# Kernel optimization log

Hardware: AMD Instinct MI355X
Metric: run time of the kernel (lower is better)

## Reference

```python
import jax, jax.numpy as jnp
import numpy as np

STATE_DIM, ACTION_DIM, HIDDEN_DIM = 12, 4, 16  # hidden_dim must equal state_dim+action_dim
LN_EPS = 1e-5


def setup_inputs() -> dict:
    key = jax.random.key(0)
    ks = jax.random.split(key, 12)
    B, T = 8192, 256
    D = STATE_DIM + ACTION_DIM  # 16
    H = HIDDEN_DIM
    s = 1.0 / np.sqrt(D)
    sh = 1.0 / np.sqrt(H)
    return {
        "initial_state": jax.random.normal(ks[0], (B, 1, STATE_DIM), jnp.float32),
        "commands": jax.random.normal(ks[1], (B, T, ACTION_DIM), jnp.float32),
        "ln_gamma": jnp.ones((D,), jnp.float32),
        "ln_beta": jnp.zeros((D,), jnp.float32),
        "W_in": jax.random.uniform(ks[2], (H, D), jnp.float32, -s, s),
        "b_in": jax.random.uniform(ks[3], (H,), jnp.float32, -s, s),
        "W_ih": jax.random.uniform(ks[4], (4 * H, D), jnp.float32, -sh, sh),  # LSTM input_size = D
        "W_hh": jax.random.uniform(ks[5], (4 * H, H), jnp.float32, -sh, sh),
        "b_ih": jax.random.uniform(ks[6], (4 * H,), jnp.float32, -sh, sh),
        "b_hh": jax.random.uniform(ks[7], (4 * H,), jnp.float32, -sh, sh),
        "W_out": jax.random.uniform(ks[8], (STATE_DIM, H), jnp.float32, -sh, sh),
        "b_out": jax.random.uniform(ks[9], (STATE_DIM,), jnp.float32, -sh, sh),
    }


def _normalize_sincos(state, cos_idx, sin_idx):
    sn, cs = state[:, sin_idx], state[:, cos_idx]
    norm = jnp.sqrt(sn * sn + cs * cs) + 1e-8
    return state.at[:, sin_idx].set(sn / norm).at[:, cos_idx].set(cs / norm)


def _forward(initial_state, commands, ln_gamma, ln_beta, W_in, b_in,
             W_ih, W_hh, b_ih, b_hh, W_out, b_out):
    B = initial_state.shape[0]
    H = W_hh.shape[1]
    state0 = initial_state[:, 0, :]  # (B, S)
    h0 = jnp.zeros((B, H), initial_state.dtype)
    c0 = jnp.zeros((B, H), initial_state.dtype)

    def step(carry, cmd_t):
        state, h, c = carry
        x = jnp.concatenate([state, cmd_t], axis=-1)          # (B, D)
        mu = jnp.mean(x, axis=-1, keepdims=True)
        var = jnp.mean((x - mu) ** 2, axis=-1, keepdims=True)
        x = (x - mu) * jax.lax.rsqrt(var + LN_EPS) * ln_gamma + ln_beta
        x = x @ W_in.T + b_in                                  # (B, H)
        gates = x @ W_ih.T + b_ih + h @ W_hh.T + b_hh          # (B, 4H)
        i, f, g, o = jnp.split(gates, 4, axis=-1)
        c = jax.nn.sigmoid(f) * c + jax.nn.sigmoid(i) * jnp.tanh(g)
        h = jax.nn.sigmoid(o) * jnp.tanh(c)
        state = state + h @ W_out.T + b_out                    # (B, S)
        state = _normalize_sincos(state, 1, 2)
        state = _normalize_sincos(state, 3, 4)
        state = _normalize_sincos(state, 5, 6)
        return (state, h, c), state

    _, outs = jax.lax.scan(step, (state0, h0, c0), jnp.swapaxes(commands, 0, 1))
    return jnp.swapaxes(outs, 0, 1)  # (B, T, S)


def reference(initial_state, commands, ln_gamma, ln_beta, W_in, b_in,
              W_ih, W_hh, b_ih, b_hh, W_out, b_out):
    return _forward(initial_state, commands, ln_gamma, ln_beta, W_in, b_in,
                    W_ih, W_hh, b_ih, b_hh, W_out, b_out)
```

## Files before the change

### kernel.cpp

```cpp
#include <hip/hip_runtime.h>

typedef float f32x2 __attribute__((ext_vector_type(2)));
typedef float f32x4 __attribute__((ext_vector_type(4)));

#define LOG2E 1.44269504088896340736f

__device__ __forceinline__ float rcp_fast(float x) { return __builtin_amdgcn_rcpf(x); }

__device__ __forceinline__ f32x2 mk2(float a, float b) { f32x2 v; v[0] = a; v[1] = b; return v; }

__device__ __forceinline__ float sigmoid_fast(float x) {
    return rcp_fast(1.0f + __builtin_amdgcn_exp2f(-LOG2E * x));
}

__device__ __forceinline__ float tanh_fast(float x) {
    float a = __builtin_fabsf(x);
    float t = __builtin_amdgcn_exp2f(-2.0f * LOG2E * a);
    float r = (1.0f - t) * rcp_fast(1.0f + t);
    return __builtin_copysignf(r, x);
}

__device__ __forceinline__ void load_pairs16(const float* p, f32x2* dst) {
    const f32x4* q4 = (const f32x4*)p;
    f32x4 a = q4[0], b = q4[1], c = q4[2], d = q4[3];
    dst[0] = __builtin_shufflevector(a, a, 0, 1);
    dst[1] = __builtin_shufflevector(a, a, 2, 3);
    dst[2] = __builtin_shufflevector(b, b, 0, 1);
    dst[3] = __builtin_shufflevector(b, b, 2, 3);
    dst[4] = __builtin_shufflevector(c, c, 0, 1);
    dst[5] = __builtin_shufflevector(c, c, 2, 3);
    dst[6] = __builtin_shufflevector(d, d, 0, 1);
    dst[7] = __builtin_shufflevector(d, d, 2, 3);
}

__global__ __launch_bounds__(64) void vm_kernel(
    const float* __restrict__ init_state,
    const float* __restrict__ commands,
    const float* __restrict__ ln_g,
    const float* __restrict__ ln_b,
    const float* __restrict__ W_in,
    const float* __restrict__ b_in,
    const float* __restrict__ W_ih,
    const float* __restrict__ W_hh,
    const float* __restrict__ b_ih,
    const float* __restrict__ b_hh,
    const float* __restrict__ W_out,
    const float* __restrict__ b_out,
    float* __restrict__ out,
    int B, int T)
{
    const int lane = threadIdx.x;
    const int j = lane & 15;
    const int g = lane >> 4;
    const int b = blockIdx.x * 4 + g;

    __shared__ float sh_x[4][20];
    __shared__ float sh_xhh[4][36];
    __shared__ float sh_hn[4][20];

    f32x2 Wg2[8];
    float wbeta;
    float sWg = 0.0f;
    {
        const float* wr = W_in + j * 16;
        float bsum = b_in[j];
        float ssum = 0.0f;
#pragma unroll
        for (int k2 = 0; k2 < 8; ++k2) {
            float w0 = wr[2 * k2], w1 = wr[2 * k2 + 1];
            float g0 = ln_g[2 * k2], g1 = ln_g[2 * k2 + 1];
            float a0 = w0 * g0, a1 = w1 * g1;
            Wg2[k2] = mk2(a0, a1);
            bsum += w0 * ln_b[2 * k2] + w1 * ln_b[2 * k2 + 1];
            ssum += a0 + a1;
        }
        wbeta = bsum;
        sWg = ssum;
    }

    f32x2 Wx[4][8], Wh[4][8];
    float gb[4];
#pragma unroll
    for (int q = 0; q < 4; ++q) {
        const float* rx = W_ih + (q * 16 + j) * 16;
        const float* rh = W_hh + (q * 16 + j) * 16;
#pragma unroll
        for (int k2 = 0; k2 < 8; ++k2) {
            Wx[q][k2] = mk2(rx[2 * k2], rx[2 * k2 + 1]);
            Wh[q][k2] = mk2(rh[2 * k2], rh[2 * k2 + 1]);
        }
        gb[q] = b_ih[q * 16 + j] + b_hh[q * 16 + j];
    }

    f32x2 Wo[8];
    float bo = 0.0f;
#pragma unroll
    for (int k2 = 0; k2 < 8; ++k2) Wo[k2] = mk2(0.0f, 0.0f);
    if (j < 12) {
        const float* ro = W_out + j * 16;
#pragma unroll
        for (int k2 = 0; k2 < 8; ++k2) Wo[k2] = mk2(ro[2 * k2], ro[2 * k2 + 1]);
        bo = b_out[j];
    }

    const bool is_state = (j < 12);
    float st = is_state ? init_state[b * 12 + j] : 0.0f;
    float h = 0.0f, c = 0.0f;

    const float* cmd_ptr = commands + (size_t)b * T * 4 + (j - 12);
    float cmd = (j >= 12) ? cmd_ptr[0] : 0.0f;

    float* out_ptr = out + (size_t)b * T * 12 + j;

    int pj = j;
    if (j >= 1 && j <= 6) pj = ((j - 1) ^ 1) + 1;
    const int psrc = (lane & 48) | pj;
    const bool donorm = (j >= 1 && j <= 6);

    for (int t = 0; t < T; ++t) {
        float x = is_state ? st : cmd;
        sh_x[g][j] = x;

        float cmd_next = 0.0f;
        {
            int tn = (t + 1 < T) ? (t + 1) : t;
            if (j >= 12) cmd_next = cmd_ptr[(size_t)tn * 4];
        }
        __syncthreads();

        f32x2 xp[8];
        load_pairs16(&sh_x[g][0], xp);

        f32x2 s2 = ((xp[0] + xp[1]) + (xp[2] + xp[3])) + ((xp[4] + xp[5]) + (xp[6] + xp[7]));
        float sum = s2[0] + s2[1];
        f32x2 q2 = xp[0] * xp[0];
#pragma unroll
        for (int k2 = 1; k2 < 8; ++k2) q2 += xp[k2] * xp[k2];
        float sumsq = q2[0] + q2[1];
        float mu = sum * 0.0625f;
        float var = sumsq * 0.0625f - mu * mu;
        float inv = __builtin_amdgcn_rsqf(var + 1e-5f);

        f32x2 d2 = Wg2[0] * xp[0];
#pragma unroll
        for (int k2 = 1; k2 < 8; ++k2) d2 += Wg2[k2] * xp[k2];
        float xh = ((d2[0] + d2[1]) - mu * sWg) * inv + wbeta;

        sh_xhh[g][j] = xh;
        sh_xhh[g][16 + j] = h;
        __syncthreads();

        f32x2 ap[8], hp[8];
        load_pairs16(&sh_xhh[g][0], ap);
        load_pairs16(&sh_xhh[g][16], hp);

        f32x2 ai = mk2(0.f, 0.f), af = mk2(0.f, 0.f), ag = mk2(0.f, 0.f), ao = mk2(0.f, 0.f);
#pragma unroll
        for (int k2 = 0; k2 < 8; ++k2) {
            f32x2 xv = ap[k2], hv = hp[k2];
            ai += Wx[0][k2] * xv; af += Wx[1][k2] * xv;
            ag += Wx[2][k2] * xv; ao += Wx[3][k2] * xv;
            ai += Wh[0][k2] * hv; af += Wh[1][k2] * hv;
            ag += Wh[2][k2] * hv; ao += Wh[3][k2] * hv;
        }
        float gi = ai[0] + ai[1] + gb[0];
        float gf = af[0] + af[1] + gb[1];
        float gg = ag[0] + ag[1] + gb[2];
        float go = ao[0] + ao[1] + gb[3];

        float iv = sigmoid_fast(gi);
        float fv = sigmoid_fast(gf);
        float gv = tanh_fast(gg);
        float ov = sigmoid_fast(go);
        c = fv * c + iv * gv;
        h = ov * tanh_fast(c);

        sh_hn[g][j] = h;
        __syncthreads();

        f32x2 hn[8];
        load_pairs16(&sh_hn[g][0], hn);
        f32x2 o2 = Wo[0] * hn[0];
#pragma unroll
        for (int k2 = 1; k2 < 8; ++k2) o2 += Wo[k2] * hn[k2];

        if (is_state) st += (o2[0] + o2[1]) + bo;

        float pv = __shfl(st, psrc, 64);
        if (donorm) {
            float n = __builtin_amdgcn_sqrtf(st * st + pv * pv) + 1e-8f;
            st *= rcp_fast(n);
        }

        if (is_state) out_ptr[0] = st;
        out_ptr += 12;
        cmd = cmd_next;
    }
}

extern "C" void kernel_launch(void* const* d_in, const int* in_sizes, int n_in,
                              void* d_out, int out_size, void* d_ws, size_t ws_size,
                              hipStream_t stream) {
    const float* init_state = (const float*)d_in[0];
    const float* commands   = (const float*)d_in[1];
    const float* ln_g       = (const float*)d_in[2];
    const float* ln_b       = (const float*)d_in[3];
    const float* W_in       = (const float*)d_in[4];
    const float* b_in       = (const float*)d_in[5];
    const float* W_ih       = (const float*)d_in[6];
    const float* W_hh       = (const float*)d_in[7];
    const float* b_ih       = (const float*)d_in[8];
    const float* b_hh       = (const float*)d_in[9];
    const float* W_out      = (const float*)d_in[10];
    const float* b_out      = (const float*)d_in[11];

    int B = in_sizes[0] / 12;
    int T = in_sizes[1] / (B * 4);

    int blocks = B / 4;
    vm_kernel<<<blocks, 64, 0, stream>>>(init_state, commands, ln_g, ln_b,
                                         W_in, b_in, W_ih, W_hh, b_ih, b_hh,
                                         W_out, b_out, (float*)d_out, B, T);
}
```

Baseline: 359.2 us.

## Replace LDS exchanges and barriers with DPP row-rotate broadcasts in LSTM step

Each batch row's 16 lanes now exchange x, h and the normalized state through DPP row_ror operations instead of shared memory plus three __syncthreads per timestep. Weights are pre-permuted per lane by the rotation index, and the input and recurrent weights are packed into f32x2 pairs so each rotation step feeds packed FMAs. This targets the per-step LDS round trips and barrier latency on the serial recurrence, at the cost of 15 DPP moves per exchange and more register pressure. Launch bounds also request 2 waves per EU.

```diff
diff --git a/kernel.cpp b/kernel.cpp
--- a/kernel.cpp
+++ b/kernel.cpp
@@ -1,13 +1,11 @@
 #include <hip/hip_runtime.h>
+#include <utility>
 
 typedef float f32x2 __attribute__((ext_vector_type(2)));
-typedef float f32x4 __attribute__((ext_vector_type(4)));
 
 #define LOG2E 1.44269504088896340736f
 
 __device__ __forceinline__ float rcp_fast(float x) { return __builtin_amdgcn_rcpf(x); }
-
-__device__ __forceinline__ f32x2 mk2(float a, float b) { f32x2 v; v[0] = a; v[1] = b; return v; }
 
 __device__ __forceinline__ float sigmoid_fast(float x) {
     return rcp_fast(1.0f + __builtin_amdgcn_exp2f(-LOG2E * x));
@@ -20,20 +18,29 @@
     return __builtin_copysignf(r, x);
 }
 
-__device__ __forceinline__ void load_pairs16(const float* p, f32x2* dst) {
-    const f32x4* q4 = (const f32x4*)p;
-    f32x4 a = q4[0], b = q4[1], c = q4[2], d = q4[3];
-    dst[0] = __builtin_shufflevector(a, a, 0, 1);
-    dst[1] = __builtin_shufflevector(a, a, 2, 3);
-    dst[2] = __builtin_shufflevector(b, b, 0, 1);
-    dst[3] = __builtin_shufflevector(b, b, 2, 3);
-    dst[4] = __builtin_shufflevector(c, c, 0, 1);
-    dst[5] = __builtin_shufflevector(c, c, 2, 3);
-    dst[6] = __builtin_shufflevector(d, d, 0, 1);
-    dst[7] = __builtin_shufflevector(d, d, 2, 3);
-}
-
-__global__ __launch_bounds__(64) void vm_kernel(
+template <int R>
+__device__ __forceinline__ int ror16_i(int v) {
+    if constexpr (R == 0) {
+        return v;
+    } else {
+        return __builtin_amdgcn_update_dpp(v, v, 0x120 + R, 0xF, 0xF, false);
+    }
+}
+template <int R>
+__device__ __forceinline__ float ror16(float v) {
+    return __builtin_bit_cast(float, ror16_i<R>(__builtin_bit_cast(int, v)));
+}
+
+template <typename F, int... Rs>
+__device__ __forceinline__ void sf_impl(F&& f, std::integer_sequence<int, Rs...>) {
+    (f(std::integral_constant<int, Rs>{}), ...);
+}
+template <int N, typename F>
+__device__ __forceinline__ void static_for(F&& f) {
+    sf_impl(f, std::make_integer_sequence<int, N>{});
+}
+
+__global__ __launch_bounds__(64, 2) void vm_kernel(
     const float* __restrict__ init_state,
     const float* __restrict__ commands,
     const float* __restrict__ ln_g,
@@ -51,57 +58,64 @@
 {
     const int lane = threadIdx.x;
     const int j = lane & 15;
-    const int g = lane >> 4;
-    const int b = blockIdx.x * 4 + g;
-
-    __shared__ float sh_x[4][20];
-    __shared__ float sh_xhh[4][36];
-    __shared__ float sh_hn[4][20];
-
-    f32x2 Wg2[8];
-    float wbeta;
-    float sWg = 0.0f;
+    const int b = blockIdx.x * 4 + (lane >> 4);
+
+    int kr[16];
+    kr[0] = j;
+    static_for<15>([&](auto rc) {
+        constexpr int R = decltype(rc)::value + 1;
+        kr[R] = ror16_i<R>(j);
+    });
+
+    float Wg[16];
+    float wbeta, sWg = 0.0f;
     {
         const float* wr = W_in + j * 16;
         float bsum = b_in[j];
-        float ssum = 0.0f;
-#pragma unroll
-        for (int k2 = 0; k2 < 8; ++k2) {
-            float w0 = wr[2 * k2], w1 = wr[2 * k2 + 1];
-            float g0 = ln_g[2 * k2], g1 = ln_g[2 * k2 + 1];
-            float a0 = w0 * g0, a1 = w1 * g1;
-            Wg2[k2] = mk2(a0, a1);
-            bsum += w0 * ln_b[2 * k2] + w1 * ln_b[2 * k2 + 1];
-            ssum += a0 + a1;
+#pragma unroll
+        for (int r = 0; r < 16; ++r) {
+            int k = kr[r];
+            float w = wr[k] * ln_g[k];
+            Wg[r] = w;
+            sWg += w;
         }
+#pragma unroll
+        for (int k = 0; k < 16; ++k) bsum += wr[k] * ln_b[k];
         wbeta = bsum;
-        sWg = ssum;
-    }
-
-    f32x2 Wx[4][8], Wh[4][8];
+    }
+
+    f32x2 Wpk[4][16];
     float gb[4];
 #pragma unroll
     for (int q = 0; q < 4; ++q) {
         const float* rx = W_ih + (q * 16 + j) * 16;
         const float* rh = W_hh + (q * 16 + j) * 16;
 #pragma unroll
-        for (int k2 = 0; k2 < 8; ++k2) {
-            Wx[q][k2] = mk2(rx[2 * k2], rx[2 * k2 + 1]);
-            Wh[q][k2] = mk2(rh[2 * k2], rh[2 * k2 + 1]);
+        for (int r = 0; r < 16; ++r) {
+            int k = kr[r];
+            f32x2 w;
+            w[0] = rx[k];
+            w[1] = rh[k];
+            Wpk[q][r] = w;
         }
         gb[q] = b_ih[q * 16 + j] + b_hh[q * 16 + j];
     }
 
-    f32x2 Wo[8];
+    float Wo[16];
     float bo = 0.0f;
 #pragma unroll
-    for (int k2 = 0; k2 < 8; ++k2) Wo[k2] = mk2(0.0f, 0.0f);
+    for (int r = 0; r < 16; ++r) Wo[r] = 0.0f;
     if (j < 12) {
         const float* ro = W_out + j * 16;
 #pragma unroll
-        for (int k2 = 0; k2 < 8; ++k2) Wo[k2] = mk2(ro[2 * k2], ro[2 * k2 + 1]);
+        for (int r = 0; r < 16; ++r) Wo[r] = ro[kr[r]];
         bo = b_out[j];
     }
+
+    int pj = j;
+    if (j >= 1 && j <= 6) pj = ((j - 1) ^ 1) + 1;
+    const bool donorm = (j >= 1 && j <= 6);
+    const bool use_r1 = (kr[1] == pj);
 
     const bool is_state = (j < 12);
     float st = is_state ? init_state[b * 12 + j] : 0.0f;
@@ -112,83 +126,68 @@
 
     float* out_ptr = out + (size_t)b * T * 12 + j;
 
-    int pj = j;
-    if (j >= 1 && j <= 6) pj = ((j - 1) ^ 1) + 1;
-    const int psrc = (lane & 48) | pj;
-    const bool donorm = (j >= 1 && j <= 6);
-
     for (int t = 0; t < T; ++t) {
         float x = is_state ? st : cmd;
-        sh_x[g][j] = x;
-
-        float cmd_next = 0.0f;
-        {
-            int tn = (t + 1 < T) ? (t + 1) : t;
-            if (j >= 12) cmd_next = cmd_ptr[(size_t)tn * 4];
-        }
-        __syncthreads();
-
-        f32x2 xp[8];
-        load_pairs16(&sh_x[g][0], xp);
-
-        f32x2 s2 = ((xp[0] + xp[1]) + (xp[2] + xp[3])) + ((xp[4] + xp[5]) + (xp[6] + xp[7]));
-        float sum = s2[0] + s2[1];
-        f32x2 q2 = xp[0] * xp[0];
-#pragma unroll
-        for (int k2 = 1; k2 < 8; ++k2) q2 += xp[k2] * xp[k2];
-        float sumsq = q2[0] + q2[1];
+
+        int tn = (t + 1 < T) ? (t + 1) : t;
+        float cmd_next = (j >= 12) ? cmd_ptr[(size_t)tn * 4] : 0.0f;
+
+        float sum = x;
+        float sumsq = x * x;
+        float dot = Wg[0] * x;
+        static_for<15>([&](auto rc) {
+            constexpr int R = decltype(rc)::value + 1;
+            float xr = ror16<R>(x);
+            sum += xr;
+            sumsq = __builtin_fmaf(xr, xr, sumsq);
+            dot = __builtin_fmaf(Wg[R], xr, dot);
+        });
         float mu = sum * 0.0625f;
-        float var = sumsq * 0.0625f - mu * mu;
+        float var = __builtin_fmaf(sumsq, 0.0625f, -mu * mu);
         float inv = __builtin_amdgcn_rsqf(var + 1e-5f);
-
-        f32x2 d2 = Wg2[0] * xp[0];
-#pragma unroll
-        for (int k2 = 1; k2 < 8; ++k2) d2 += Wg2[k2] * xp[k2];
-        float xh = ((d2[0] + d2[1]) - mu * sWg) * inv + wbeta;
-
-        sh_xhh[g][j] = xh;
-        sh_xhh[g][16 + j] = h;
-        __syncthreads();
-
-        f32x2 ap[8], hp[8];
-        load_pairs16(&sh_xhh[g][0], ap);
-        load_pairs16(&sh_xhh[g][16], hp);
-
-        f32x2 ai = mk2(0.f, 0.f), af = mk2(0.f, 0.f), ag = mk2(0.f, 0.f), ao = mk2(0.f, 0.f);
-#pragma unroll
-        for (int k2 = 0; k2 < 8; ++k2) {
-            f32x2 xv = ap[k2], hv = hp[k2];
-            ai += Wx[0][k2] * xv; af += Wx[1][k2] * xv;
-            ag += Wx[2][k2] * xv; ao += Wx[3][k2] * xv;
-            ai += Wh[0][k2] * hv; af += Wh[1][k2] * hv;
-            ag += Wh[2][k2] * hv; ao += Wh[3][k2] * hv;
-        }
-        float gi = ai[0] + ai[1] + gb[0];
-        float gf = af[0] + af[1] + gb[1];
-        float gg = ag[0] + ag[1] + gb[2];
-        float go = ao[0] + ao[1] + gb[3];
+        float xh = __builtin_fmaf(dot - mu * sWg, inv, wbeta);
+
+        f32x2 v0;
+        v0[0] = xh;
+        v0[1] = h;
+        f32x2 a0 = Wpk[0][0] * v0;
+        f32x2 a1 = Wpk[1][0] * v0;
+        f32x2 a2 = Wpk[2][0] * v0;
+        f32x2 a3 = Wpk[3][0] * v0;
+        static_for<15>([&](auto rc) {
+            constexpr int R = decltype(rc)::value + 1;
+            f32x2 v;
+            v[0] = ror16<R>(xh);
+            v[1] = ror16<R>(h);
+            a0 += Wpk[0][R] * v;
+            a1 += Wpk[1][R] * v;
+            a2 += Wpk[2][R] * v;
+            a3 += Wpk[3][R] * v;
+        });
+        float gi = a0[0] + a0[1] + gb[0];
+        float gf = a1[0] + a1[1] + gb[1];
+        float gg = a2[0] + a2[1] + gb[2];
+        float go = a3[0] + a3[1] + gb[3];
 
         float iv = sigmoid_fast(gi);
         float fv = sigmoid_fast(gf);
         float gv = tanh_fast(gg);
         float ov = sigmoid_fast(go);
-        c = fv * c + iv * gv;
+        c = __builtin_fmaf(fv, c, iv * gv);
         h = ov * tanh_fast(c);
 
-        sh_hn[g][j] = h;
-        __syncthreads();
-
-        f32x2 hn[8];
-        load_pairs16(&sh_hn[g][0], hn);
-        f32x2 o2 = Wo[0] * hn[0];
-#pragma unroll
-        for (int k2 = 1; k2 < 8; ++k2) o2 += Wo[k2] * hn[k2];
-
-        if (is_state) st += (o2[0] + o2[1]) + bo;
-
-        float pv = __shfl(st, psrc, 64);
+        float o = Wo[0] * h;
+        static_for<15>([&](auto rc) {
+            constexpr int R = decltype(rc)::value + 1;
+            o = __builtin_fmaf(Wo[R], ror16<R>(h), o);
+        });
+        if (is_state) st += o + bo;
+
+        float p1 = ror16<1>(st);
+        float p15 = ror16<15>(st);
+        float pv = use_r1 ? p1 : p15;
         if (donorm) {
-            float n = __builtin_amdgcn_sqrtf(st * st + pv * pv) + 1e-8f;
+            float n = __builtin_amdgcn_sqrtf(__builtin_fmaf(st, st, pv * pv)) + 1e-8f;
             st *= rcp_fast(n);
         }
 
```

Result: slower. 450.1 us (+25.3%).

## Fold LayerNorm and input projection into LSTM gates and split gates across half-waves

Applied to the files above, without the earlier changes.

Precomputes the product of W_ih with the gamma-scaled W_in, so the gate preactivations come straight from the raw input with a mean-correction term. This removes the separate input-projection matmul and one barrier per step. Each sample now uses 32 lanes, each computing two gates, and the halves swap gates through ds_swizzle. W_out moves to shared memory, the sin/cos partner shuffle becomes DPP row rotates, and the block handles 2 samples instead of 4, which doubles the number of blocks but does redundant work in the upper half-wave.

```diff
diff --git a/kernel.cpp b/kernel.cpp
--- a/kernel.cpp
+++ b/kernel.cpp
@@ -6,13 +6,12 @@
 #define LOG2E 1.44269504088896340736f
 
 __device__ __forceinline__ float rcp_fast(float x) { return __builtin_amdgcn_rcpf(x); }
-
 __device__ __forceinline__ f32x2 mk2(float a, float b) { f32x2 v; v[0] = a; v[1] = b; return v; }
+__device__ __forceinline__ f32x2 splat2(float a) { return mk2(a, a); }
 
 __device__ __forceinline__ float sigmoid_fast(float x) {
     return rcp_fast(1.0f + __builtin_amdgcn_exp2f(-LOG2E * x));
 }
-
 __device__ __forceinline__ float tanh_fast(float x) {
     float a = __builtin_fabsf(x);
     float t = __builtin_amdgcn_exp2f(-2.0f * LOG2E * a);
@@ -20,7 +19,21 @@
     return __builtin_copysignf(r, x);
 }
 
-__device__ __forceinline__ void load_pairs16(const float* p, f32x2* dst) {
+__device__ __forceinline__ float swz_xor16(float v) {
+    return __builtin_bit_cast(float, __builtin_amdgcn_ds_swizzle(__builtin_bit_cast(int, v), 0x401F));
+}
+
+template <int R>
+__device__ __forceinline__ int ror16_i(int v) {
+    if constexpr (R == 0) return v;
+    else return __builtin_amdgcn_update_dpp(v, v, 0x120 + R, 0xF, 0xF, false);
+}
+template <int R>
+__device__ __forceinline__ float ror16(float v) {
+    return __builtin_bit_cast(float, ror16_i<R>(__builtin_bit_cast(int, v)));
+}
+
+__device__ __forceinline__ void quads_to_pairs(const float* p, f32x2* dst) {
     const f32x4* q4 = (const f32x4*)p;
     f32x4 a = q4[0], b = q4[1], c = q4[2], d = q4[3];
     dst[0] = __builtin_shufflevector(a, a, 0, 1);
@@ -33,7 +46,7 @@
     dst[7] = __builtin_shufflevector(d, d, 2, 3);
 }
 
-__global__ __launch_bounds__(64) void vm_kernel(
+__global__ __launch_bounds__(64, 4) void vm_kernel(
     const float* __restrict__ init_state,
     const float* __restrict__ commands,
     const float* __restrict__ ln_g,
@@ -51,148 +64,153 @@
 {
     const int lane = threadIdx.x;
     const int j = lane & 15;
-    const int g = lane >> 4;
-    const int b = blockIdx.x * 4 + g;
-
-    __shared__ float sh_x[4][20];
-    __shared__ float sh_xhh[4][36];
-    __shared__ float sh_hn[4][20];
-
-    f32x2 Wg2[8];
-    float wbeta;
-    float sWg = 0.0f;
+    const int u = (lane >> 4) & 1;
+    const int g = lane >> 5;
+    const int b = blockIdx.x * 2 + g;
+
+    __shared__ __align__(16) float sh_x[2][16];
+    __shared__ __align__(16) float sh_h[2][16];
+    __shared__ __align__(16) float sh_wo[16][20];
+
+    if (lane < 16) {
+#pragma unroll
+        for (int k = 0; k < 16; ++k)
+            sh_wo[lane][k] = (lane < 12) ? W_out[lane * 16 + k] : 0.0f;
+    }
+
+    const int Q0 = (2 * u) * 16 + j;
+    const int Q1 = Q0 + 16;
+
+    f32x2 A0[8], A1[8];
+#pragma unroll
+    for (int k = 0; k < 8; ++k) { A0[k] = splat2(0.0f); A1[k] = splat2(0.0f); }
+    float uu0 = 0.0f, uu1 = 0.0f;
+    float d0 = b_ih[Q0] + b_hh[Q0];
+    float d1 = b_ih[Q1] + b_hh[Q1];
+
+    for (int m = 0; m < 16; ++m) {
+        float wi0 = W_ih[Q0 * 16 + m];
+        float wi1 = W_ih[Q1 * 16 + m];
+        const float* wr = W_in + m * 16;
+        float sW = 0.0f, wb = b_in[m];
+#pragma unroll
+        for (int k = 0; k < 8; ++k) {
+            float g0 = wr[2 * k] * ln_g[2 * k];
+            float g1 = wr[2 * k + 1] * ln_g[2 * k + 1];
+            f32x2 wg = mk2(g0, g1);
+            A0[k] += splat2(wi0) * wg;
+            A1[k] += splat2(wi1) * wg;
+            sW += g0 + g1;
+            wb += wr[2 * k] * ln_b[2 * k] + wr[2 * k + 1] * ln_b[2 * k + 1];
+        }
+        uu0 += wi0 * sW; uu1 += wi1 * sW;
+        d0 += wi0 * wb;  d1 += wi1 * wb;
+    }
+
+    f32x2 Wh0[8], Wh1[8];
     {
-        const float* wr = W_in + j * 16;
-        float bsum = b_in[j];
-        float ssum = 0.0f;
-#pragma unroll
-        for (int k2 = 0; k2 < 8; ++k2) {
-            float w0 = wr[2 * k2], w1 = wr[2 * k2 + 1];
-            float g0 = ln_g[2 * k2], g1 = ln_g[2 * k2 + 1];
-            float a0 = w0 * g0, a1 = w1 * g1;
-            Wg2[k2] = mk2(a0, a1);
-            bsum += w0 * ln_b[2 * k2] + w1 * ln_b[2 * k2 + 1];
-            ssum += a0 + a1;
-        }
-        wbeta = bsum;
-        sWg = ssum;
-    }
-
-    f32x2 Wx[4][8], Wh[4][8];
-    float gb[4];
-#pragma unroll
-    for (int q = 0; q < 4; ++q) {
-        const float* rx = W_ih + (q * 16 + j) * 16;
-        const float* rh = W_hh + (q * 16 + j) * 16;
-#pragma unroll
-        for (int k2 = 0; k2 < 8; ++k2) {
-            Wx[q][k2] = mk2(rx[2 * k2], rx[2 * k2 + 1]);
-            Wh[q][k2] = mk2(rh[2 * k2], rh[2 * k2 + 1]);
-        }
-        gb[q] = b_ih[q * 16 + j] + b_hh[q * 16 + j];
-    }
-
-    f32x2 Wo[8];
-    float bo = 0.0f;
-#pragma unroll
-    for (int k2 = 0; k2 < 8; ++k2) Wo[k2] = mk2(0.0f, 0.0f);
-    if (j < 12) {
-        const float* ro = W_out + j * 16;
-#pragma unroll
-        for (int k2 = 0; k2 < 8; ++k2) Wo[k2] = mk2(ro[2 * k2], ro[2 * k2 + 1]);
-        bo = b_out[j];
-    }
-
-    const bool is_state = (j < 12);
-    float st = is_state ? init_state[b * 12 + j] : 0.0f;
-    float h = 0.0f, c = 0.0f;
+        const float* r0 = W_hh + Q0 * 16;
+        const float* r1 = W_hh + Q1 * 16;
+#pragma unroll
+        for (int k = 0; k < 8; ++k) {
+            Wh0[k] = mk2(r0[2 * k], r0[2 * k + 1]);
+            Wh1[k] = mk2(r1[2 * k], r1[2 * k + 1]);
+        }
+    }
+
+    const float bo = (j < 12) ? b_out[j] : 0.0f;
+
+    float st = (j < 12) ? init_state[b * 12 + j] : 0.0f;
+    float c = 0.0f, h = 0.0f;
+    f32x2 hp[8];
+#pragma unroll
+    for (int k = 0; k < 8; ++k) hp[k] = splat2(0.0f);
 
     const float* cmd_ptr = commands + (size_t)b * T * 4 + (j - 12);
     float cmd = (j >= 12) ? cmd_ptr[0] : 0.0f;
-
     float* out_ptr = out + (size_t)b * T * 12 + j;
 
     int pj = j;
     if (j >= 1 && j <= 6) pj = ((j - 1) ^ 1) + 1;
-    const int psrc = (lane & 48) | pj;
     const bool donorm = (j >= 1 && j <= 6);
+    const bool use_r1 = (ror16_i<1>(j) == pj);
+
+    __syncthreads();
 
     for (int t = 0; t < T; ++t) {
-        float x = is_state ? st : cmd;
-        sh_x[g][j] = x;
-
-        float cmd_next = 0.0f;
-        {
-            int tn = (t + 1 < T) ? (t + 1) : t;
-            if (j >= 12) cmd_next = cmd_ptr[(size_t)tn * 4];
-        }
+        float x = (j < 12) ? st : cmd;
+        if (u == 0) sh_x[g][j] = x;
+
+        int tn = (t + 1 < T) ? (t + 1) : t;
+        float cmd_next = (j >= 12) ? cmd_ptr[(size_t)tn * 4] : 0.0f;
+
         __syncthreads();
 
         f32x2 xp[8];
-        load_pairs16(&sh_x[g][0], xp);
+        quads_to_pairs(&sh_x[g][0], xp);
 
         f32x2 s2 = ((xp[0] + xp[1]) + (xp[2] + xp[3])) + ((xp[4] + xp[5]) + (xp[6] + xp[7]));
         float sum = s2[0] + s2[1];
         f32x2 q2 = xp[0] * xp[0];
 #pragma unroll
-        for (int k2 = 1; k2 < 8; ++k2) q2 += xp[k2] * xp[k2];
+        for (int k = 1; k < 8; ++k) q2 += xp[k] * xp[k];
         float sumsq = q2[0] + q2[1];
         float mu = sum * 0.0625f;
-        float var = sumsq * 0.0625f - mu * mu;
+        float var = __builtin_fmaf(sumsq, 0.0625f, -mu * mu);
         float inv = __builtin_amdgcn_rsqf(var + 1e-5f);
 
-        f32x2 d2 = Wg2[0] * xp[0];
-#pragma unroll
-        for (int k2 = 1; k2 < 8; ++k2) d2 += Wg2[k2] * xp[k2];
-        float xh = ((d2[0] + d2[1]) - mu * sWg) * inv + wbeta;
-
-        sh_xhh[g][j] = xh;
-        sh_xhh[g][16 + j] = h;
-        __syncthreads();
-
-        f32x2 ap[8], hp[8];
-        load_pairs16(&sh_xhh[g][0], ap);
-        load_pairs16(&sh_xhh[g][16], hp);
-
-        f32x2 ai = mk2(0.f, 0.f), af = mk2(0.f, 0.f), ag = mk2(0.f, 0.f), ao = mk2(0.f, 0.f);
-#pragma unroll
-        for (int k2 = 0; k2 < 8; ++k2) {
-            f32x2 xv = ap[k2], hv = hp[k2];
-            ai += Wx[0][k2] * xv; af += Wx[1][k2] * xv;
-            ag += Wx[2][k2] * xv; ao += Wx[3][k2] * xv;
-            ai += Wh[0][k2] * hv; af += Wh[1][k2] * hv;
-            ag += Wh[2][k2] * hv; ao += Wh[3][k2] * hv;
-        }
-        float gi = ai[0] + ai[1] + gb[0];
-        float gf = af[0] + af[1] + gb[1];
-        float gg = ag[0] + ag[1] + gb[2];
-        float go = ao[0] + ao[1] + gb[3];
+        f32x2 a0 = A0[0] * xp[0], a1 = A1[0] * xp[0];
+        f32x2 h0 = Wh0[0] * hp[0], h1 = Wh1[0] * hp[0];
+#pragma unroll
+        for (int k = 1; k < 8; ++k) {
+            a0 += A0[k] * xp[k];
+            a1 += A1[k] * xp[k];
+            h0 += Wh0[k] * hp[k];
+            h1 += Wh1[k] * hp[k];
+        }
+        float gx0 = a0[0] + a0[1], gx1 = a1[0] + a1[1];
+        float gh0 = h0[0] + h0[1], gh1 = h1[0] + h1[1];
+
+        float G0 = __builtin_fmaf(__builtin_fmaf(-mu, uu0, gx0), inv, d0 + gh0);
+        float G1 = __builtin_fmaf(__builtin_fmaf(-mu, uu1, gx1), inv, d1 + gh1);
+
+        float e0 = swz_xor16(G0);
+        float e1 = swz_xor16(G1);
+        float gi = u ? e0 : G0;
+        float gf = u ? e1 : G1;
+        float gg = u ? G0 : e0;
+        float go = u ? G1 : e1;
 
         float iv = sigmoid_fast(gi);
         float fv = sigmoid_fast(gf);
         float gv = tanh_fast(gg);
         float ov = sigmoid_fast(go);
-        c = fv * c + iv * gv;
+        c = __builtin_fmaf(fv, c, iv * gv);
         h = ov * tanh_fast(c);
 
-        sh_hn[g][j] = h;
+        if (u == 0) sh_h[g][j] = h;
         __syncthreads();
 
-        f32x2 hn[8];
-        load_pairs16(&sh_hn[g][0], hn);
-        f32x2 o2 = Wo[0] * hn[0];
-#pragma unroll
-        for (int k2 = 1; k2 < 8; ++k2) o2 += Wo[k2] * hn[k2];
-
-        if (is_state) st += (o2[0] + o2[1]) + bo;
-
-        float pv = __shfl(st, psrc, 64);
+        quads_to_pairs(&sh_h[g][0], hp);
+
+        f32x2 wop[8];
+        quads_to_pairs(&sh_wo[j][0], wop);
+        f32x2 oa = wop[0] * hp[0];
+#pragma unroll
+        for (int k = 1; k < 8; ++k) oa += wop[k] * hp[k];
+        float o = oa[0] + oa[1];
+
+        st += o + bo;
+
+        float p1 = ror16<1>(st);
+        float p15 = ror16<15>(st);
+        float pv = use_r1 ? p1 : p15;
         if (donorm) {
-            float n = __builtin_amdgcn_sqrtf(st * st + pv * pv) + 1e-8f;
+            float n = __builtin_amdgcn_sqrtf(__builtin_fmaf(st, st, pv * pv)) + 1e-8f;
             st *= rcp_fast(n);
         }
 
-        if (is_state) out_ptr[0] = st;
+        if (u == 0 && j < 12) out_ptr[0] = st;
         out_ptr += 12;
         cmd = cmd_next;
     }
@@ -217,7 +235,7 @@
     int B = in_sizes[0] / 12;
     int T = in_sizes[1] / (B * 4);
 
-    int blocks = B / 4;
+    int blocks = B / 2;
     vm_kernel<<<blocks, 64, 0, stream>>>(init_state, commands, ln_g, ln_b,
                                          W_in, b_in, W_ih, W_hh, b_ih, b_hh,
                                          W_out, b_out, (float*)d_out, B, T);
```

Result: slower. 427.7 us (+19.1%).
